# Kernel tuning notes

Hardware: AMD Instinct MI355X
Metric: run time of the kernel (lower is better)

Reference implementation:

```python
import jax, jax.numpy as jnp
import numpy as np

B, S, D = 32, 4096, 512  # batch, src seq len, hidden (n_hidden_in == n_hidden_out)


def setup_inputs() -> dict:
    key = jax.random.key(0)
    k1, k2, k3, k4 = jax.random.split(key, 4)
    return {
        "hidden_targ": jax.random.normal(k1, (B, D), dtype=jnp.float32),
        "hidden_src": jax.random.normal(k2, (B, S, D), dtype=jnp.float32),
        "mask": jnp.ones((B, S), dtype=jnp.float32),
        "W": jax.random.normal(k3, (D, 2 * D), dtype=jnp.float32) * (2 * D) ** -0.5,
        "V": jax.random.uniform(k4, (D,), dtype=jnp.float32),
    }


def reference(hidden_targ, hidden_src, mask, W, V):
    # W @ cat(targ, src) == targ @ Wt^T + src @ Ws^T  (avoids materializing the
    # repeated/concatenated [b, s, 2d] tensor the torch code builds)
    d = hidden_targ.shape[-1]
    Wt, Ws = W[:, :d], W[:, d:]
    # [b, 1, h] + [b, s, h] -> tanh pre-activation
    pre = jnp.tanh(
        jnp.einsum("bd,hd->bh", hidden_targ, Wt)[:, None, :]
        + jnp.einsum("bsd,hd->bsh", hidden_src, Ws)
    )
    e = jnp.einsum("bsh,h->bs", pre, V)            # scores [b, s]
    att_weights = jax.nn.softmax(e, axis=1) * mask  # softmax then mask (as in source)
    ctx = jnp.einsum("bs,bsd->bd", att_weights, hidden_src)
    hidden_output = ctx + hidden_targ
    return att_weights, hidden_output
```

## Files before the change

### kernel.cpp

```cpp
#include <hip/hip_runtime.h>
#include <hip/hip_bf16.h>


typedef __attribute__((ext_vector_type(8))) short bf16x8;
typedef __attribute__((ext_vector_type(4))) float f32x4;

#define L2E 1.4426950408889634f

static __device__ __forceinline__ unsigned cvt2(float a, float b) {
    union { __hip_bfloat162 h; unsigned u; } v;
    v.h = __float22bfloat162_rn(make_float2(a, b));
    return v.u;
}
static __device__ __forceinline__ float bits2f(unsigned u) {
    union { unsigned u; float f; } x; x.u = u; return x.f;
}
static __device__ __forceinline__ float fast_tanh(float x) {
    float ex = exp2f(x * 2.8853900817779268f);
    return 1.0f - 2.0f / (ex + 1.0f);
}

#define WS_WBF   0L
#define WS_T     524288L
#define WS_E     589824L
#define WS_MST   1114112L
#define WS_CTXP  1130496L

__global__ void prep_kernel(const float* __restrict__ W,
                            const float* __restrict__ targ,
                            short* __restrict__ wbf,
                            float* __restrict__ t) {
    if (blockIdx.x < 128) {
        const int gid = blockIdx.x * 256 + threadIdx.x;
        const int tile = gid >> 9, p = gid & 511;
        const int hx = tile >> 4, ktile = tile & 15;
        const int r = p >> 2, up = p & 3;
        const int u = up ^ ((r >> 1) & 3);
        const float* s = W + (long)(hx * 128 + r) * 1024 + 512 + ktile * 32 + u * 8;
        float4 v0 = *(const float4*)(s);
        float4 v1 = *(const float4*)(s + 4);
        uint4 pk;
        pk.x = cvt2(v0.x, v0.y); pk.y = cvt2(v0.z, v0.w);
        pk.z = cvt2(v1.x, v1.y); pk.w = cvt2(v1.z, v1.w);
        ((uint4*)wbf)[gid] = pk;
        return;
    }
    __shared__ float tg[512];
    const int bid = blockIdx.x - 128;
    const int b = bid >> 2;
    const int hbase = (bid & 3) * 128;
    const int tid = threadIdx.x;
    tg[tid]       = targ[b * 512 + tid];
    tg[tid + 256] = targ[b * 512 + tid + 256];
    __syncthreads();
    const int lane = tid & 63, wave = tid >> 6;
    for (int h = hbase + wave; h < hbase + 128; h += 4) {
        const float* wr = W + (long)h * 1024;
        float s = 0.f;
        #pragma unroll
        for (int i = 0; i < 2; i++) {
            const int d = lane * 4 + i * 256;
            float4 wv = *(const float4*)(wr + d);
            s += wv.x * tg[d] + wv.y * tg[d + 1] + wv.z * tg[d + 2] + wv.w * tg[d + 3];
        }
        s += __shfl_xor(s, 1);  s += __shfl_xor(s, 2);  s += __shfl_xor(s, 4);
        s += __shfl_xor(s, 8);  s += __shfl_xor(s, 16); s += __shfl_xor(s, 32);
        if (lane == 0) t[b * 512 + h] = s;
    }
}

__global__ __launch_bounds__(256, 2)
void fused_kernel(const float* __restrict__ src,
                  const short* __restrict__ wbf,
                  const float* __restrict__ t,
                  const float* __restrict__ V,
                  const float* __restrict__ mask,
                  float* __restrict__ e_ws,
                  float* __restrict__ mstats,
                  float* __restrict__ ctxp) {
    __shared__ __align__(16) short As[64 * 512];
    __shared__ float er[4][64];
    __shared__ float pbuf[64];

    const int tid = threadIdx.x;
    const int mt  = blockIdx.x;
    const int b   = mt >> 6;
    const long m0 = (long)mt * 64;

    const int lane = tid & 63, wave = tid >> 6;
    const int lr = lane & 15, quad = lane >> 4;
    const int l7 = lr & 7;

    {
        const int row = tid >> 2, cp4 = tid & 3, r7 = row & 7;
        const float* ap = src + (m0 + row) * 512;
        short* abase = As + row * 512;
        #pragma unroll
        for (int j = 0; j < 16; ++j) {
            const int kb = j * 32 + cp4 * 8;
            f32x4 v0 = __builtin_nontemporal_load((const f32x4*)(ap + kb));
            f32x4 v1 = __builtin_nontemporal_load((const f32x4*)(ap + kb + 4));
            uint4 pk;
            pk.x = cvt2(v0.x, v0.y); pk.y = cvt2(v0.z, v0.w);
            pk.z = cvt2(v1.x, v1.y); pk.w = cvt2(v1.z, v1.w);
            *(uint4*)(abase + (((j * 4 + cp4) ^ r7) * 8)) = pk;
        }
    }
    __syncthreads();

    const short* bstream = wbf + (long)wave * 16 * 4096;
    int boff[8];
    #pragma unroll
    for (int ni = 0; ni < 8; ++ni) {
        const int row = ni * 16 + lr;
        boff[ni] = row * 32 + (quad ^ ((row >> 1) & 3)) * 8;
    }

    f32x4 acc[4][8];
    #pragma unroll
    for (int mi = 0; mi < 4; ++mi)
        #pragma unroll
        for (int ni = 0; ni < 8; ++ni)
            acc[mi][ni] = (f32x4){0.f, 0.f, 0.f, 0.f};

    bf16x8 b0[8], b1[8], af[4];
    #pragma unroll
    for (int ni = 0; ni < 8; ++ni)
        b0[ni] = *(const bf16x8*)(bstream + boff[ni]);

    #pragma unroll
    for (int kt = 0; kt < 16; kt += 2) {
        #pragma unroll
        for (int ni = 0; ni < 4; ++ni)
            b1[ni] = *(const bf16x8*)(bstream + (kt + 1) * 4096 + boff[ni]);
        #pragma unroll
        for (int mi = 0; mi < 4; ++mi)
            af[mi] = *(const bf16x8*)(As + (mi * 16 + lr) * 512 +
                                      (((kt * 4 + quad) ^ l7) * 8));
        #pragma unroll
        for (int mi = 0; mi < 4; ++mi)
            #pragma unroll
            for (int ni = 0; ni < 4; ++ni)
                acc[mi][ni] = __builtin_amdgcn_mfma_f32_16x16x32_bf16(
                    af[mi], b0[ni], acc[mi][ni], 0, 0, 0);
        #pragma unroll
        for (int ni = 4; ni < 8; ++ni)
            b1[ni] = *(const bf16x8*)(bstream + (kt + 1) * 4096 + boff[ni]);
        #pragma unroll
        for (int mi = 0; mi < 4; ++mi)
            #pragma unroll
            for (int ni = 4; ni < 8; ++ni)
                acc[mi][ni] = __builtin_amdgcn_mfma_f32_16x16x32_bf16(
                    af[mi], b0[ni], acc[mi][ni], 0, 0, 0);

        if (kt + 2 < 16) {
            #pragma unroll
            for (int ni = 0; ni < 4; ++ni)
                b0[ni] = *(const bf16x8*)(bstream + (kt + 2) * 4096 + boff[ni]);
        }
        #pragma unroll
        for (int mi = 0; mi < 4; ++mi)
            af[mi] = *(const bf16x8*)(As + (mi * 16 + lr) * 512 +
                                      ((((kt + 1) * 4 + quad) ^ l7) * 8));
        #pragma unroll
        for (int mi = 0; mi < 4; ++mi)
            #pragma unroll
            for (int ni = 0; ni < 4; ++ni)
                acc[mi][ni] = __builtin_amdgcn_mfma_f32_16x16x32_bf16(
                    af[mi], b1[ni], acc[mi][ni], 0, 0, 0);
        if (kt + 2 < 16) {
            #pragma unroll
            for (int ni = 4; ni < 8; ++ni)
                b0[ni] = *(const bf16x8*)(bstream + (kt + 2) * 4096 + boff[ni]);
        }
        #pragma unroll
        for (int mi = 0; mi < 4; ++mi)
            #pragma unroll
            for (int ni = 4; ni < 8; ++ni)
                acc[mi][ni] = __builtin_amdgcn_mfma_f32_16x16x32_bf16(
                    af[mi], b1[ni], acc[mi][ni], 0, 0, 0);
    }

    const float* trow = t + b * 512;
    float th[8], vv[8];
    #pragma unroll
    for (int ni = 0; ni < 8; ++ni) {
        const int h = wave * 128 + ni * 16 + lr;
        th[ni] = trow[h];
        vv[ni] = V[h];
    }
    #pragma unroll
    for (int mi = 0; mi < 4; ++mi) {
        #pragma unroll
        for (int r = 0; r < 4; ++r) {
            float es = 0.f;
            #pragma unroll
            for (int ni = 0; ni < 8; ++ni)
                es += fast_tanh(acc[mi][ni][r] + th[ni]) * vv[ni];
            es += __shfl_xor(es, 1);
            es += __shfl_xor(es, 2);
            es += __shfl_xor(es, 4);
            es += __shfl_xor(es, 8);
            if (lr == 0) er[wave][mi * 16 + quad * 4 + r] = es;
        }
    }
    __syncthreads();

    if (tid < 64) {
        const float myE = er[0][tid] + er[1][tid] + er[2][tid] + er[3][tid];
        float mx = myE;
        #pragma unroll
        for (int m = 1; m <= 32; m <<= 1) mx = fmaxf(mx, __shfl_xor(mx, m));
        const float pv = exp2f((myE - mx) * L2E);
        float sv = pv;
        #pragma unroll
        for (int m = 1; m <= 32; m <<= 1) sv += __shfl_xor(sv, m);
        e_ws[m0 + tid] = myE;
        pbuf[tid] = pv * mask[m0 + tid];
        if (tid == 0) { mstats[mt * 2] = mx; mstats[mt * 2 + 1] = sv; }
    }
    __syncthreads();

    const int d0 = tid * 2;
    const int cb = d0 >> 3, coff = d0 & 7;
    float a0 = 0.f, a1 = 0.f;
    #pragma unroll 8
    for (int s = 0; s < 64; ++s) {
        const unsigned u = *(const unsigned*)(As + s * 512 + ((cb ^ (s & 7)) * 8) + coff);
        const float w = pbuf[s];
        a0 += w * bits2f(u << 16);
        a1 += w * bits2f(u & 0xffff0000u);
    }
    ctxp[(long)mt * 512 + d0]     = a0;
    ctxp[(long)mt * 512 + d0 + 1] = a1;
}

__global__ void final2_kernel(const float* __restrict__ e_ws,
                              const float* __restrict__ mstats,
                              const float* __restrict__ ctxp,
                              const float* __restrict__ mask,
                              const float* __restrict__ targ,
                              float* __restrict__ att,
                              float* __restrict__ outh) {
    const int b = blockIdx.x, tid = threadIdx.x;
    __shared__ float wL[64];
    __shared__ float bc[2];
    if (tid < 64) {
        const float mv = mstats[(b * 64 + tid) * 2];
        const float sv = mstats[(b * 64 + tid) * 2 + 1];
        float M = mv;
        #pragma unroll
        for (int m = 1; m <= 32; m <<= 1) M = fmaxf(M, __shfl_xor(M, m));
        float sc = sv * exp2f((mv - M) * L2E);
        #pragma unroll
        for (int m = 1; m <= 32; m <<= 1) sc += __shfl_xor(sc, m);
        wL[tid] = exp2f((mv - M) * L2E) / sc;
        if (tid == 0) { bc[0] = M; bc[1] = sc; }
    }
    __syncthreads();
    const float M = bc[0], invS = 1.0f / bc[1];
    #pragma unroll
    for (int i = 0; i < 16; i++) {
        const int s = i * 256 + tid;
        const long idx = (long)b * 4096 + s;
        att[idx] = exp2f((e_ws[idx] - M) * L2E) * invS * mask[idx];
    }
    #pragma unroll
    for (int dd = 0; dd < 2; dd++) {
        const int d = dd * 256 + tid;
        float a = targ[b * 512 + d];
        #pragma unroll 4
        for (int L = 0; L < 64; L++)
            a += wL[L] * ctxp[((long)(b * 64 + L)) * 512 + d];
        outh[b * 512 + d] = a;
    }
}

extern "C" void kernel_launch(void* const* d_in, const int* in_sizes, int n_in,
                              void* d_out, int out_size, void* d_ws, size_t ws_size,
                              hipStream_t stream) {
    const float* targ = (const float*)d_in[0];
    const float* src  = (const float*)d_in[1];
    const float* mask = (const float*)d_in[2];
    const float* W    = (const float*)d_in[3];
    const float* V    = (const float*)d_in[4];

    float* att  = (float*)d_out;
    float* outh = (float*)d_out + 131072;

    char* ws = (char*)d_ws;
    short* wbf   = (short*)(ws + WS_WBF);
    float* t     = (float*)(ws + WS_T);
    float* e     = (float*)(ws + WS_E);
    float* mst   = (float*)(ws + WS_MST);
    float* ctxp  = (float*)(ws + WS_CTXP);

    prep_kernel<<<256, 256, 0, stream>>>(W, targ, wbf, t);
    fused_kernel<<<2048, 256, 0, stream>>>(src, wbf, t, V, mask, e, mst, ctxp);
    final2_kernel<<<32, 256, 0, stream>>>(e, mst, ctxp, mask, targ, att, outh);
}
```

Baseline: 465.1 us.

## Double fused kernel to 512 threads, splitting H across 8 waves

```diff
diff --git a/kernel.cpp b/kernel.cpp
--- a/kernel.cpp
+++ b/kernel.cpp
@@ -15,9 +15,12 @@
 static __device__ __forceinline__ float bits2f(unsigned u) {
     union { unsigned u; float f; } x; x.u = u; return x.f;
 }
+static __device__ __forceinline__ float fast_exp2(float x) {
+    return __builtin_amdgcn_exp2f(x);
+}
 static __device__ __forceinline__ float fast_tanh(float x) {
-    float ex = exp2f(x * 2.8853900817779268f);
-    return 1.0f - 2.0f / (ex + 1.0f);
+    float ex = __builtin_amdgcn_exp2f(x * 2.8853900817779268f);
+    return 1.0f - 2.0f * __builtin_amdgcn_rcpf(ex + 1.0f);
 }
 
 #define WS_WBF   0L
@@ -69,7 +72,7 @@
     }
 }
 
-__global__ __launch_bounds__(256, 2)
+__global__ __launch_bounds__(512, 4)
 void fused_kernel(const float* __restrict__ src,
                   const short* __restrict__ wbf,
                   const float* __restrict__ t,
@@ -79,8 +82,9 @@
                   float* __restrict__ mstats,
                   float* __restrict__ ctxp) {
     __shared__ __align__(16) short As[64 * 512];
-    __shared__ float er[4][64];
+    __shared__ float er[8][64];
     __shared__ float pbuf[64];
+    __shared__ float cbuf[512];
 
     const int tid = threadIdx.x;
     const int mt  = blockIdx.x;
@@ -92,100 +96,78 @@
     const int l7 = lr & 7;
 
     {
-        const int row = tid >> 2, cp4 = tid & 3, r7 = row & 7;
+        const int row = tid >> 3, cp8 = tid & 7, r7 = row & 7;
         const float* ap = src + (m0 + row) * 512;
         short* abase = As + row * 512;
         #pragma unroll
-        for (int j = 0; j < 16; ++j) {
-            const int kb = j * 32 + cp4 * 8;
+        for (int j = 0; j < 8; ++j) {
+            const int kb = j * 64 + cp8 * 8;
             f32x4 v0 = __builtin_nontemporal_load((const f32x4*)(ap + kb));
             f32x4 v1 = __builtin_nontemporal_load((const f32x4*)(ap + kb + 4));
             uint4 pk;
             pk.x = cvt2(v0.x, v0.y); pk.y = cvt2(v0.z, v0.w);
             pk.z = cvt2(v1.x, v1.y); pk.w = cvt2(v1.z, v1.w);
-            *(uint4*)(abase + (((j * 4 + cp4) ^ r7) * 8)) = pk;
-        }
-    }
-    __syncthreads();
-
-    const short* bstream = wbf + (long)wave * 16 * 4096;
-    int boff[8];
-    #pragma unroll
-    for (int ni = 0; ni < 8; ++ni) {
-        const int row = ni * 16 + lr;
-        boff[ni] = row * 32 + (quad ^ ((row >> 1) & 3)) * 8;
-    }
-
-    f32x4 acc[4][8];
+            *(uint4*)(abase + (((j * 8 + cp8) ^ r7) * 8)) = pk;
+        }
+    }
+    __syncthreads();
+
+    const short* bstream = wbf + (long)(wave >> 1) * 16 * 4096;
+    const int rbase = (wave & 1) * 64;
+    const short* bptr[4];
+    #pragma unroll
+    for (int ni = 0; ni < 4; ++ni) {
+        const int row = rbase + ni * 16 + lr;
+        bptr[ni] = bstream + row * 32 + (quad ^ ((row >> 1) & 3)) * 8;
+    }
+
+    f32x4 acc[4][4];
     #pragma unroll
     for (int mi = 0; mi < 4; ++mi)
         #pragma unroll
-        for (int ni = 0; ni < 8; ++ni)
+        for (int ni = 0; ni < 4; ++ni)
             acc[mi][ni] = (f32x4){0.f, 0.f, 0.f, 0.f};
 
-    bf16x8 b0[8], b1[8], af[4];
-    #pragma unroll
-    for (int ni = 0; ni < 8; ++ni)
-        b0[ni] = *(const bf16x8*)(bstream + boff[ni]);
+    bf16x8 b0[4], b1[4];
+    #pragma unroll
+    for (int ni = 0; ni < 4; ++ni)
+        b0[ni] = *(const bf16x8*)(bptr[ni]);
 
     #pragma unroll
     for (int kt = 0; kt < 16; kt += 2) {
         #pragma unroll
         for (int ni = 0; ni < 4; ++ni)
-            b1[ni] = *(const bf16x8*)(bstream + (kt + 1) * 4096 + boff[ni]);
-        #pragma unroll
-        for (int mi = 0; mi < 4; ++mi)
-            af[mi] = *(const bf16x8*)(As + (mi * 16 + lr) * 512 +
-                                      (((kt * 4 + quad) ^ l7) * 8));
-        #pragma unroll
-        for (int mi = 0; mi < 4; ++mi)
+            b1[ni] = *(const bf16x8*)(bptr[ni] + (kt + 1) * 4096);
+        #pragma unroll
+        for (int mi = 0; mi < 4; ++mi) {
+            bf16x8 af = *(const bf16x8*)(As + (mi * 16 + lr) * 512 +
+                                         (((kt * 4 + quad) ^ l7) * 8));
             #pragma unroll
             for (int ni = 0; ni < 4; ++ni)
                 acc[mi][ni] = __builtin_amdgcn_mfma_f32_16x16x32_bf16(
-                    af[mi], b0[ni], acc[mi][ni], 0, 0, 0);
-        #pragma unroll
-        for (int ni = 4; ni < 8; ++ni)
-            b1[ni] = *(const bf16x8*)(bstream + (kt + 1) * 4096 + boff[ni]);
-        #pragma unroll
-        for (int mi = 0; mi < 4; ++mi)
-            #pragma unroll
-            for (int ni = 4; ni < 8; ++ni)
+                    af, b0[ni], acc[mi][ni], 0, 0, 0);
+        }
+        if (kt + 2 < 16) {
+            #pragma unroll
+            for (int ni = 0; ni < 4; ++ni)
+                b0[ni] = *(const bf16x8*)(bptr[ni] + (kt + 2) * 4096);
+        }
+        #pragma unroll
+        for (int mi = 0; mi < 4; ++mi) {
+            bf16x8 af = *(const bf16x8*)(As + (mi * 16 + lr) * 512 +
+                                         ((((kt + 1) * 4 + quad) ^ l7) * 8));
+            #pragma unroll
+            for (int ni = 0; ni < 4; ++ni)
                 acc[mi][ni] = __builtin_amdgcn_mfma_f32_16x16x32_bf16(
-                    af[mi], b0[ni], acc[mi][ni], 0, 0, 0);
-
-        if (kt + 2 < 16) {
-            #pragma unroll
-            for (int ni = 0; ni < 4; ++ni)
-                b0[ni] = *(const bf16x8*)(bstream + (kt + 2) * 4096 + boff[ni]);
-        }
-        #pragma unroll
-        for (int mi = 0; mi < 4; ++mi)
-            af[mi] = *(const bf16x8*)(As + (mi * 16 + lr) * 512 +
-                                      ((((kt + 1) * 4 + quad) ^ l7) * 8));
-        #pragma unroll
-        for (int mi = 0; mi < 4; ++mi)
-            #pragma unroll
-            for (int ni = 0; ni < 4; ++ni)
-                acc[mi][ni] = __builtin_amdgcn_mfma_f32_16x16x32_bf16(
-                    af[mi], b1[ni], acc[mi][ni], 0, 0, 0);
-        if (kt + 2 < 16) {
-            #pragma unroll
-            for (int ni = 4; ni < 8; ++ni)
-                b0[ni] = *(const bf16x8*)(bstream + (kt + 2) * 4096 + boff[ni]);
-        }
-        #pragma unroll
-        for (int mi = 0; mi < 4; ++mi)
-            #pragma unroll
-            for (int ni = 4; ni < 8; ++ni)
-                acc[mi][ni] = __builtin_amdgcn_mfma_f32_16x16x32_bf16(
-                    af[mi], b1[ni], acc[mi][ni], 0, 0, 0);
+                    af, b1[ni], acc[mi][ni], 0, 0, 0);
+        }
     }
 
     const float* trow = t + b * 512;
-    float th[8], vv[8];
-    #pragma unroll
-    for (int ni = 0; ni < 8; ++ni) {
-        const int h = wave * 128 + ni * 16 + lr;
+    float th[4], vv[4];
+    #pragma unroll
+    for (int ni = 0; ni < 4; ++ni) {
+        const int h = wave * 64 + ni * 16 + lr;
         th[ni] = trow[h];
         vv[ni] = V[h];
     }
@@ -195,7 +177,7 @@
         for (int r = 0; r < 4; ++r) {
             float es = 0.f;
             #pragma unroll
-            for (int ni = 0; ni < 8; ++ni)
+            for (int ni = 0; ni < 4; ++ni)
                 es += fast_tanh(acc[mi][ni][r] + th[ni]) * vv[ni];
             es += __shfl_xor(es, 1);
             es += __shfl_xor(es, 2);
@@ -207,11 +189,12 @@
     __syncthreads();
 
     if (tid < 64) {
-        const float myE = er[0][tid] + er[1][tid] + er[2][tid] + er[3][tid];
+        float myE = er[0][tid] + er[1][tid] + er[2][tid] + er[3][tid]
+                  + er[4][tid] + er[5][tid] + er[6][tid] + er[7][tid];
         float mx = myE;
         #pragma unroll
         for (int m = 1; m <= 32; m <<= 1) mx = fmaxf(mx, __shfl_xor(mx, m));
-        const float pv = exp2f((myE - mx) * L2E);
+        const float pv = fast_exp2((myE - mx) * L2E);
         float sv = pv;
         #pragma unroll
         for (int m = 1; m <= 32; m <<= 1) sv += __shfl_xor(sv, m);
@@ -221,18 +204,25 @@
     }
     __syncthreads();
 
-    const int d0 = tid * 2;
+    const int sg = tid >> 8;
+    const int d0 = (tid & 255) * 2;
     const int cb = d0 >> 3, coff = d0 & 7;
     float a0 = 0.f, a1 = 0.f;
     #pragma unroll 8
-    for (int s = 0; s < 64; ++s) {
+    for (int s = sg * 32; s < sg * 32 + 32; ++s) {
         const unsigned u = *(const unsigned*)(As + s * 512 + ((cb ^ (s & 7)) * 8) + coff);
         const float w = pbuf[s];
         a0 += w * bits2f(u << 16);
         a1 += w * bits2f(u & 0xffff0000u);
     }
-    ctxp[(long)mt * 512 + d0]     = a0;
-    ctxp[(long)mt * 512 + d0 + 1] = a1;
+    if (sg) { cbuf[d0] = a0; cbuf[d0 + 1] = a1; }
+    __syncthreads();
+    if (!sg) {
+        a0 += cbuf[d0];
+        a1 += cbuf[d0 + 1];
+        ctxp[(long)mt * 512 + d0]     = a0;
+        ctxp[(long)mt * 512 + d0 + 1] = a1;
+    }
 }
 
 __global__ void final2_kernel(const float* __restrict__ e_ws,
@@ -296,6 +286,6 @@
     float* ctxp  = (float*)(ws + WS_CTXP);
 
     prep_kernel<<<256, 256, 0, stream>>>(W, targ, wbf, t);
-    fused_kernel<<<2048, 256, 0, stream>>>(src, wbf, t, V, mask, e, mst, ctxp);
+    fused_kernel<<<2048, 512, 0, stream>>>(src, wbf, t, V, mask, e, mst, ctxp);
     final2_kernel<<<32, 256, 0, stream>>>(e, mst, ctxp, mask, targ, att, outh);
 }
```

New measurement: 454.4 us. 2.3% less time.
